# Performance work log

Measured on AMD Instinct MI355X. Metric: run time of the kernel, lower is better.

Reference implementation:

```python
import jax, jax.numpy as jnp
import numpy as np
from jax import lax

B, T = 512, 64
IN, H, V1, P = 256, 512, 101, 8  # input_size, rnn_size, vocab_size+1, max_param
CLS, REG = 512, 512


def setup_inputs() -> dict:
    key = jax.random.key(0)
    ks = jax.random.split(key, 20)
    u = lambda k, s: jax.random.uniform(k, s, jnp.float32, -0.1, 0.1)
    sh = 1.0 / np.sqrt(H)
    ul = lambda k, s: jax.random.uniform(k, s, jnp.float32, -sh, sh)
    return {
        "x": jax.random.normal(ks[0], (B, IN), jnp.float32),
        "y": jax.random.randint(ks[1], (B, T), 0, V1),
        "embed": u(ks[2], (V1, IN)),
        "w_ih0": ul(ks[3], (4 * H, IN)),
        "w_hh0": ul(ks[4], (4 * H, H)),
        "w_ih1": ul(ks[5], (4 * H, H)),
        "w_hh1": ul(ks[6], (4 * H, H)),
        "l1w": u(ks[7], (CLS, H)), "l1b": jnp.zeros((CLS,), jnp.float32),
        "l2w": u(ks[8], (V1, CLS)), "l2b": jnp.zeros((V1,), jnp.float32),
        "r1w": u(ks[9], (REG, H)), "r1b": jnp.zeros((REG,), jnp.float32),
        "r2w": u(ks[10], (V1 * P, V1 + REG)), "r2b": jnp.zeros((V1 * P,), jnp.float32),
    }


def _cell(xi, h, c, wih, whh):
    g = xi @ wih.T + h @ whh.T          # [B, 4H], gate order i,f,g,o (no bias)
    i, f, gg, o = jnp.split(g, 4, axis=-1)
    c = jax.nn.sigmoid(f) * c + jax.nn.sigmoid(i) * jnp.tanh(gg)
    h = jax.nn.sigmoid(o) * jnp.tanh(c)
    return h, c


def reference(x, y, embed, w_ih0, w_hh0, w_ih1, w_hh1,
              l1w, l1b, l2w, l2b, r1w, r1b, r2w, r2b):
    # teacher forcing (sample_prob=0): step-0 input is x, step-i input is embed(y[:, i-1])
    emb = embed[y[:, :-1]]                                  # [B, T-1, IN]
    xt = jnp.concatenate([x[None], jnp.transpose(emb, (1, 0, 2))], axis=0)  # [T, B, IN]

    z = jnp.zeros((x.shape[0], H), x.dtype)

    def step(carry, xi):
        h0, c0, h1, c1 = carry
        h0, c0 = _cell(xi, h0, c0, w_ih0, w_hh0)
        h1, c1 = _cell(h0, h1, c1, w_ih1, w_hh1)
        return (h0, c0, h1, c1), h1

    _, outs = lax.scan(step, (z, z, z, z), xt)              # [T, B, H]

    feat2 = jax.nn.relu(outs @ l1w.T + l1b) @ l2w.T + l2b   # [T, B, V1]
    pgm_score = jax.nn.log_softmax(feat2, axis=-1)
    trans_prob = lax.stop_gradient(jax.nn.softmax(feat2, axis=-1))
    pf1 = jax.nn.relu(outs @ r1w.T + r1b)                   # [T, B, REG]
    ps = (jnp.concatenate([trans_prob, pf1], axis=-1) @ r2w.T + r2b)
    ps = ps.reshape(T, -1, V1, P)                           # [T, B, V1, P]
    idx = y.T                                               # [T, B]
    param = ps[jnp.arange(T)[:, None], jnp.arange(x.shape[0])[None, :], idx]  # [T, B, P]
    return (jnp.transpose(pgm_score, (1, 0, 2)),            # [B, T, V1]
            jnp.transpose(param, (1, 0, 2)))                # [B, T, P]
```

## Files before the change

### kernel.cpp

```cpp
#include <hip/hip_runtime.h>
#include <stdint.h>

typedef unsigned short u16;
typedef short bf16x8 __attribute__((ext_vector_type(8)));
typedef float f32x4 __attribute__((ext_vector_type(4)));
typedef int i32x4 __attribute__((ext_vector_type(4)));

#define DEV static __device__ __forceinline__

constexpr int B_ = 512, T_ = 64, IN_ = 256, H_ = 512, V1_ = 101, P_ = 8, G4_ = 2048;
constexpr int EXR = 613;
constexpr int M_  = T_ * B_;
constexpr int NBLK = 256;

DEV float b2f(u16 u) { union { uint32_t i; float f; } v; v.i = ((uint32_t)u) << 16; return v.f; }
DEV u16 f2b(float f) {
  union { float f; uint32_t i; } v; v.f = f;
  uint32_t i = v.i;
  return (u16)((i + 0x7fffu + ((i >> 16) & 1u)) >> 16);
}
DEV float sigf(float x) { return 1.f / (1.f + __expf(-x)); }
DEV float tanh_(float x) {
  float c = fminf(fmaxf(x, -15.f), 15.f);
  float e = __expf(2.f * c);
  return (e - 1.f) / (e + 1.f);
}
DEV bf16x8 ld8(const u16* p) { return *reinterpret_cast<const bf16x8*>(p); }
DEV f32x4 mfma16(bf16x8 a, bf16x8 b, f32x4 c) {
  return __builtin_amdgcn_mfma_f32_16x16x32_bf16(a, b, c, 0, 0, 0);
}

struct CvtArgs {
  const float* src[9];
  u16* dst[9];
  int pre[10];
};

__global__ __launch_bounds__(256) void k_cvtall(CvtArgs a) {
  int gid = blockIdx.x * 256 + threadIdx.x;
  if (gid >= a.pre[9]) return;
  int s = 0;
#pragma unroll
  for (int i = 1; i < 9; ++i) s += (gid >= a.pre[i]);
  const int local = gid - a.pre[s];
  const float4 v = reinterpret_cast<const float4*>(a.src[s])[local];
  ushort4 o;
  o.x = f2b(v.x); o.y = f2b(v.y); o.z = f2b(v.z); o.w = f2b(v.w);
  reinterpret_cast<ushort4*>(a.dst[s])[local] = o;
}

__global__ __launch_bounds__(256) void k_precomp(const u16* __restrict__ ex_src,
                                                 const u16* __restrict__ wih0b,
                                                 float* __restrict__ EX0) {
  const int lane = threadIdx.x & 63;
  const int wv = threadIdx.x >> 6;
  const int m0 = blockIdx.x * 64 + wv * 16;
  const int n0 = blockIdx.y * 64;
  const int lr = lane & 15;
  const int lk = (lane >> 4) * 8;

  const int arow = m0 + lr;
  const bool valid = arow < EXR;

  f32x4 acc[4] = {};
  for (int k0 = 0; k0 < IN_; k0 += 32) {
    bf16x8 a = {};
    if (valid) a = ld8(ex_src + (size_t)arow * IN_ + k0 + lk);
#pragma unroll
    for (int c = 0; c < 4; ++c) {
      bf16x8 b = ld8(wih0b + (size_t)(n0 + c * 16 + lr) * IN_ + k0 + lk);
      acc[c] = mfma16(a, b, acc[c]);
    }
  }
  const int rb = (lane >> 4) * 4;
#pragma unroll
  for (int c = 0; c < 4; ++c)
#pragma unroll
    for (int r = 0; r < 4; ++r) {
      int row = m0 + rb + r;
      int col = n0 + c * 16 + (lane & 15);
      if (row < EXR) EX0[(size_t)row * G4_ + col] = acc[c][r];
    }
}

__global__ __launch_bounds__(512, 1) void k_scan(
    const u16* __restrict__ whh0, const u16* __restrict__ wih1, const u16* __restrict__ whh1,
    const float* __restrict__ EX0, const int* __restrict__ y,
    u16* h0buf, u16* h1buf, unsigned* flags ) {
  __shared__ u16 h0s[16 * 512];
  __shared__ u16 h1s[16 * 512];
  __shared__ u16 stage0[16][64];
  __shared__ u16 stage1[16][64];
  const size_t BH = (size_t)B_ * H_;
  const int tid = threadIdx.x;
  const int lane = tid & 63;
  const int wv = tid >> 6;
  const int q = wv & 3;
  const bool isL1 = wv >= 4;
  const int bm = blockIdx.x >> 3;
  const int bj = blockIdx.x & 7;
  const int lr = lane & 15;
  const int lk = (lane >> 4) * 8;
  const int col = bj * 64 + q * 16 + lr;
  const int rb = (lane >> 4) * 4;
  const int lcol = q * 16 + lr;

  const u16* wp[8];
#pragma unroll
  for (int g = 0; g < 4; ++g) {
    if (!isL1) {
      wp[g] = whh0 + (size_t)(g * H_ + col) * H_ + lk;
      wp[4 + g] = whh0 + (size_t)(g * H_ + col) * H_ + lk;
    } else {
      wp[g] = wih1 + (size_t)(g * H_ + col) * H_ + lk;
      wp[4 + g] = whh1 + (size_t)(g * H_ + col) * H_ + lk;
    }
  }
  f32x4 cst = {};
  unsigned* gflags = flags + bm * 16;

  for (int k = 0; k <= T_; ++k) {
    {
      const u16* h0g = h0buf + (size_t)k * BH + (size_t)(bm * 16) * H_;
#pragma unroll
      for (int rr = 0; rr < 2; ++rr) {
        const int idx = rr * 512 + tid;
        const int row = idx >> 6, cc = idx & 63;
        i32x4 d = *(const i32x4*)(h0g + (size_t)row * H_ + cc * 8);
        *(i32x4*)((char*)h0s + row * 1024 + ((cc * 16) ^ ((row & 7) << 4))) = d;
      }
      if (k >= 1) {
        const u16* h1g = h1buf + (size_t)(k - 1) * BH + (size_t)(bm * 16) * H_;
#pragma unroll
        for (int rr = 0; rr < 2; ++rr) {
          const int idx = rr * 512 + tid;
          const int row = idx >> 6, cc = idx & 63;
          i32x4 d = *(const i32x4*)(h1g + (size_t)row * H_ + cc * 8);
          *(i32x4*)((char*)h1s + row * 1024 + ((cc * 16) ^ ((row & 7) << 4))) = d;
        }
      }
    }
    __syncthreads();

    if (!isL1) {
      if (k < T_) {
        float ex[4][4];
#pragma unroll
        for (int r = 0; r < 4; ++r) {
          const int row = bm * 16 + rb + r;
          const int srow = (k == 0) ? (V1_ + row) : y[row * T_ + k - 1];
          const float* bp = EX0 + (size_t)srow * G4_ + col;
#pragma unroll
          for (int g = 0; g < 4; ++g) ex[g][r] = bp[(size_t)g * H_];
        }
        bf16x8 wf0[4], wf1[4], wf2[4];
#pragma unroll
        for (int g = 0; g < 4; ++g) {
          wf0[g] = ld8(wp[g]);
          wf1[g] = ld8(wp[g] + 32);
          wf2[g] = ld8(wp[g] + 64);
        }
        f32x4 acc[4] = {};
#pragma unroll
        for (int i = 0; i < 16; ++i) {
          bf16x8 a0 = *(const bf16x8*)((const char*)h0s + lr * 1024 + (((i * 32 + lk) * 2) ^ ((lr & 7) << 4)));
          bf16x8 cur[4];
#pragma unroll
          for (int g = 0; g < 4; ++g)
            cur[g] = (i % 3 == 0) ? wf0[g] : (i % 3 == 1) ? wf1[g] : wf2[g];
          if (i + 3 < 16) {
#pragma unroll
            for (int g = 0; g < 4; ++g) {
              bf16x8 nv = ld8(wp[g] + (i + 3) * 32);
              if (i % 3 == 0) wf0[g] = nv; else if (i % 3 == 1) wf1[g] = nv; else wf2[g] = nv;
            }
          }
#pragma unroll
          for (int g = 0; g < 4; ++g) acc[g] = mfma16(a0, cur[g], acc[g]);
        }
#pragma unroll
        for (int r = 0; r < 4; ++r) {
          float iv = acc[0][r] + ex[0][r], fv = acc[1][r] + ex[1][r];
          float gv = acc[2][r] + ex[2][r], ov = acc[3][r] + ex[3][r];
          float cn = sigf(fv) * cst[r] + sigf(iv) * tanh_(gv);
          cst[r] = cn;
          stage0[rb + r][lcol] = f2b(sigf(ov) * tanh_(cn));
        }
      }
    } else {
      if (k >= 1) {
        bf16x8 wa0[4], wa1[4], wa2[4], wb0[4], wb1[4], wb2[4];
#pragma unroll
        for (int g = 0; g < 4; ++g) {
          wa0[g] = ld8(wp[g]);       wb0[g] = ld8(wp[4 + g]);
          wa1[g] = ld8(wp[g] + 32);  wb1[g] = ld8(wp[4 + g] + 32);
          wa2[g] = ld8(wp[g] + 64);  wb2[g] = ld8(wp[4 + g] + 64);
        }
        f32x4 acc[4] = {};
#pragma unroll
        for (int i = 0; i < 16; ++i) {
          const int so = ((i * 32 + lk) * 2) ^ ((lr & 7) << 4);
          bf16x8 a0 = *(const bf16x8*)((const char*)h0s + lr * 1024 + so);
          bf16x8 a1 = *(const bf16x8*)((const char*)h1s + lr * 1024 + so);
          bf16x8 ca[4], cb[4];
#pragma unroll
          for (int g = 0; g < 4; ++g) {
            ca[g] = (i % 3 == 0) ? wa0[g] : (i % 3 == 1) ? wa1[g] : wa2[g];
            cb[g] = (i % 3 == 0) ? wb0[g] : (i % 3 == 1) ? wb1[g] : wb2[g];
          }
          if (i + 3 < 16) {
#pragma unroll
            for (int g = 0; g < 4; ++g) {
              bf16x8 na = ld8(wp[g] + (i + 3) * 32);
              bf16x8 nb = ld8(wp[4 + g] + (i + 3) * 32);
              if (i % 3 == 0) { wa0[g] = na; wb0[g] = nb; }
              else if (i % 3 == 1) { wa1[g] = na; wb1[g] = nb; }
              else { wa2[g] = na; wb2[g] = nb; }
            }
          }
#pragma unroll
          for (int g = 0; g < 4; ++g) {
            acc[g] = mfma16(a0, ca[g], acc[g]);
            acc[g] = mfma16(a1, cb[g], acc[g]);
          }
        }
#pragma unroll
        for (int r = 0; r < 4; ++r) {
          float cn = sigf(acc[1][r]) * cst[r] + sigf(acc[0][r]) * tanh_(acc[2][r]);
          cst[r] = cn;
          stage1[rb + r][lcol] = f2b(sigf(acc[3][r]) * tanh_(cn));
        }
      }
    }
    __syncthreads();

    if (tid < 256) {
      if (tid < 128) {
        if (k < T_) {
          const int lrow = tid >> 3, c8 = (tid & 7) * 8;
          i32x4 d = *(const i32x4*)&stage0[lrow][c8];
          u16* gp = h0buf + (size_t)(k + 1) * BH + (size_t)(bm * 16 + lrow) * H_ + bj * 64 + c8;
          asm volatile("global_store_dwordx4 %0, %1, off sc0 sc1" :: "v"(gp), "v"(d) : "memory");
        }
      } else {
        if (k >= 1) {
          const int t2 = tid - 128;
          const int lrow = t2 >> 3, c8 = (t2 & 7) * 8;
          i32x4 d = *(const i32x4*)&stage1[lrow][c8];
          u16* gp = h1buf + (size_t)k * BH + (size_t)(bm * 16 + lrow) * H_ + bj * 64 + c8;
          asm volatile("global_store_dwordx4 %0, %1, off sc0 sc1" :: "v"(gp), "v"(d) : "memory");
        }
      }
    }
    asm volatile("s_waitcnt vmcnt(0)" ::: "memory");
    __syncthreads();
    if (wv == 0) {
      const unsigned tgt = (unsigned)(k + 1);
      if (lane == 0)
        __hip_atomic_store(&gflags[bj], tgt, __ATOMIC_RELAXED, __HIP_MEMORY_SCOPE_AGENT);
      for (;;) {
        unsigned v = __hip_atomic_load(&gflags[lane & 7], __ATOMIC_RELAXED, __HIP_MEMORY_SCOPE_AGENT);
        if (__all(v >= tgt)) break;
        __builtin_amdgcn_s_sleep(1);
      }
    }
    __syncthreads();
    asm volatile("" ::: "memory");
  }
}

__global__ __launch_bounds__(256) void k_fused1(const u16* __restrict__ outs,
                                                const u16* __restrict__ l1w, const float* __restrict__ l1b,
                                                const u16* __restrict__ r1w, const float* __restrict__ r1b,
                                                u16* __restrict__ feat1, u16* __restrict__ pf1) {
  const int lane = threadIdx.x & 63;
  const int wv = threadIdx.x >> 6;
  const int lr = lane & 15;
  const int lk = (lane >> 4) * 8;
  const int ar = blockIdx.x * 64 + wv * 16 + lr;
  const int rb = (lane >> 4) * 4;
  const int row0 = blockIdx.x * 64 + wv * 16 + rb;

  bf16x8 a[16];
  {
    const u16* ap = outs + (size_t)ar * H_ + lk;
#pragma unroll
    for (int i = 0; i < 16; ++i) a[i] = ld8(ap + i * 32);
  }
  for (int w = 0; w < 2; ++w) {
    const u16* W = w ? r1w : l1w;
    const float* bias = w ? r1b : l1b;
    u16* dst = w ? pf1 : feat1;
    for (int nc = 0; nc < 4; ++nc) {
      const u16* wr[8];
#pragma unroll
      for (int n = 0; n < 8; ++n)
        wr[n] = W + (size_t)(nc * 128 + n * 16 + lr) * H_ + lk;
      bf16x8 wcur[8];
#pragma unroll
      for (int n = 0; n < 8; ++n) wcur[n] = ld8(wr[n]);
      f32x4 acc[8] = {};
#pragma unroll
      for (int i = 0; i < 16; ++i) {
        bf16x8 wnext[8];
        if (i < 15) {
#pragma unroll
          for (int n = 0; n < 8; ++n) wnext[n] = ld8(wr[n] + (i + 1) * 32);
        }
#pragma unroll
        for (int n = 0; n < 8; ++n) acc[n] = mfma16(a[i], wcur[n], acc[n]);
        if (i < 15) {
#pragma unroll
          for (int n = 0; n < 8; ++n) wcur[n] = wnext[n];
        }
      }
#pragma unroll
      for (int n = 0; n < 8; ++n) {
        const int colc = nc * 128 + n * 16 + lr;
        const float bv = bias[colc];
#pragma unroll
        for (int r = 0; r < 4; ++r)
          dst[(size_t)(row0 + r) * H_ + colc] = f2b(fmaxf(acc[n][r] + bv, 0.f));
      }
    }
  }
}

__global__ __launch_bounds__(256) void k_fused2(const u16* __restrict__ feat1,
                                                const u16* __restrict__ l2w, const float* __restrict__ l2b,
                                                const u16* __restrict__ pf1,
                                                const float* __restrict__ r2w, const float* __restrict__ r2b,
                                                const int* __restrict__ y,
                                                float* __restrict__ pgm, float* __restrict__ par) {
  __shared__ float trans[64][104];
  const int lane = threadIdx.x & 63;
  const int wv = threadIdx.x >> 6;
  const int lr = lane & 15;
  const int lk = (lane >> 4) * 8;
  const int ar = blockIdx.x * 64 + wv * 16 + lr;
  const int rb = (lane >> 4) * 4;

  f32x4 acc[7] = {};
  {
    const u16* ap = feat1 + (size_t)ar * H_ + lk;
#pragma unroll
    for (int i = 0; i < 16; ++i) {
      bf16x8 av = ld8(ap + i * 32);
#pragma unroll
      for (int c = 0; c < 7; ++c) {
        const int n = c * 16 + lr;
        bf16x8 b = {};
        if (n < V1_) b = ld8(l2w + (size_t)n * H_ + i * 32 + lk);
        acc[c] = mfma16(av, b, acc[c]);
      }
    }
  }
#pragma unroll
  for (int r = 0; r < 4; ++r) {
    float v[7];
    float mx = -1e30f;
#pragma unroll
    for (int c = 0; c < 7; ++c) {
      const int colc = c * 16 + lr;
      v[c] = (colc < V1_) ? acc[c][r] + l2b[colc] : -1e30f;
      mx = fmaxf(mx, v[c]);
    }
#pragma unroll
    for (int o = 1; o < 16; o <<= 1) mx = fmaxf(mx, __shfl_xor(mx, o, 64));
    float e[7], s = 0.f;
#pragma unroll
    for (int c = 0; c < 7; ++c) { e[c] = (c * 16 + lr < V1_) ? __expf(v[c] - mx) : 0.f; s += e[c]; }
#pragma unroll
    for (int o = 1; o < 16; o <<= 1) s += __shfl_xor(s, o, 64);
    const float lz = __logf(s), inv = 1.f / s;
    const int m = blockIdx.x * 64 + wv * 16 + rb + r;
    const int t = m >> 9, bb = m & 511;
    float* po = pgm + ((size_t)bb * T_ + t) * V1_;
#pragma unroll
    for (int c = 0; c < 7; ++c) {
      const int colc = c * 16 + lr;
      if (colc < V1_) { po[colc] = v[c] - mx - lz; trans[wv * 16 + rb + r][colc] = e[c] * inv; }
    }
  }
  __syncthreads();
  for (int rr = 0; rr < 16; ++rr) {
    const int m = blockIdx.x * 64 + wv * 16 + rr;
    const int t = m >> 9, bb = m & 511;
    const int idx = y[bb * T_ + t];
    const float* wb = r2w + (size_t)idx * P_ * 613;
    float a8[P_] = {};
    for (int kk = lane; kk < 613; kk += 64) {
      float xv = (kk < V1_) ? trans[wv * 16 + rr][kk] : b2f(pf1[(size_t)m * H_ + kk - V1_]);
#pragma unroll
      for (int p = 0; p < P_; ++p) a8[p] += xv * wb[(size_t)p * 613 + kk];
    }
#pragma unroll
    for (int p = 0; p < P_; ++p)
#pragma unroll
      for (int o = 1; o < 64; o <<= 1) a8[p] += __shfl_xor(a8[p], o, 64);
    if (lane < P_) par[((size_t)bb * T_ + t) * P_ + lane] = a8[lane] + r2b[idx * P_ + lane];
  }
}

extern "C" void kernel_launch(void* const* d_in, const int* in_sizes, int n_in,
                              void* d_out, int out_size, void* d_ws, size_t ws_size,
                              hipStream_t stream) {
  (void)in_sizes; (void)n_in; (void)out_size; (void)ws_size;
  const float* x     = (const float*)d_in[0];
  const int*   y     = (const int*)d_in[1];
  const float* embed = (const float*)d_in[2];
  const float* wih0  = (const float*)d_in[3];
  const float* whh0  = (const float*)d_in[4];
  const float* wih1  = (const float*)d_in[5];
  const float* whh1  = (const float*)d_in[6];
  const float* l1w   = (const float*)d_in[7];
  const float* l1b   = (const float*)d_in[8];
  const float* l2w   = (const float*)d_in[9];
  const float* l2b   = (const float*)d_in[10];
  const float* r1w   = (const float*)d_in[11];
  const float* r1b   = (const float*)d_in[12];
  const float* r2w   = (const float*)d_in[13];
  const float* r2b   = (const float*)d_in[14];

  float* out_pgm = (float*)d_out;
  float* out_par = out_pgm + (size_t)B_ * T_ * V1_;

  char* ws = (char*)d_ws;
  size_t off = 0;
  auto alloc = [&](size_t bytes) { void* p = ws + off; off += (bytes + 255) & ~(size_t)255; return p; };

  const size_t BH2 = (size_t)B_ * H_ * 2;

  unsigned* flags = (unsigned*)alloc(32 * 16 * 4);
  u16* h0buf  = (u16*)alloc((size_t)(T_ + 1) * BH2);
  u16* h1buf  = (u16*)alloc((size_t)(T_ + 1) * BH2);

  float* EX0   = (float*)alloc((size_t)EXR * G4_ * 4);
  u16* ex_src  = (u16*)alloc((size_t)EXR * IN_ * 2);
  u16* wih0b   = (u16*)alloc((size_t)4 * H_ * IN_ * 2);
  u16* whh0b   = (u16*)alloc((size_t)4 * H_ * H_ * 2);
  u16* wih1b   = (u16*)alloc((size_t)4 * H_ * H_ * 2);
  u16* whh1b   = (u16*)alloc((size_t)4 * H_ * H_ * 2);
  u16* l1wb    = (u16*)alloc((size_t)H_ * H_ * 2);
  u16* r1wb    = (u16*)alloc((size_t)H_ * H_ * 2);
  u16* l2wb    = (u16*)alloc((size_t)V1_ * H_ * 2);
  u16* feat1   = (u16*)alloc((size_t)M_ * H_ * 2);
  u16* pf1     = (u16*)alloc((size_t)M_ * H_ * 2);

  (void)hipMemsetAsync(flags, 0, 32 * 16 * 4 + BH2, stream);
  (void)hipMemsetAsync(h1buf, 0, BH2, stream);

  CvtArgs ca;
  const float* srcs[9] = {embed, x, wih0, whh0, wih1, whh1, l1w, r1w, l2w};
  u16* dsts[9] = {ex_src, ex_src + (size_t)V1_ * IN_, wih0b, whh0b, wih1b, whh1b, l1wb, r1wb, l2wb};
  int ns[9] = {V1_ * IN_, B_ * IN_, 4 * H_ * IN_, 4 * H_ * H_, 4 * H_ * H_, 4 * H_ * H_,
               H_ * H_, H_ * H_, V1_ * H_};
  int acc4 = 0;
  for (int i = 0; i < 9; ++i) {
    ca.src[i] = srcs[i]; ca.dst[i] = dsts[i]; ca.pre[i] = acc4; acc4 += ns[i] / 4;
  }
  ca.pre[9] = acc4;
  k_cvtall<<<(acc4 + 255) / 256, 256, 0, stream>>>(ca);

  k_precomp<<<dim3(10, 32), 256, 0, stream>>>(ex_src, wih0b, EX0);

  k_scan<<<NBLK, 512, 0, stream>>>(whh0b, wih1b, whh1b, EX0, y, h0buf, h1buf, flags);

  u16* outs = h1buf + (size_t)B_ * H_;
  k_fused1<<<512, 256, 0, stream>>>(outs, l1wb, l1b, r1wb, r1b, feat1, pf1);
  k_fused2<<<512, 256, 0, stream>>>(feat1, l2wb, l2b, pf1, r2w, r2b, y, out_pgm, out_par);
}
```

Before: 1.934 ms.

## Fuse tail MLP kernels and keep intermediates in swizzled shared memory

Merges the two post-scan kernels into one, so the ReLU hidden features for the classifier and regressor branches stay in LDS instead of going through global memory. XOR swizzling on the LDS rows is meant to avoid bank conflicts when the MFMA loads read them back. This removes one kernel launch and the global write and read of two 32K×512 bf16 buffers. In exchange it uses 128KB of LDS per block, which limits occupancy to one block per CU.

```diff
diff --git a/kernel.cpp b/kernel.cpp
--- a/kernel.cpp
+++ b/kernel.cpp
@@ -269,17 +269,23 @@
   }
 }
 
-__global__ __launch_bounds__(256) void k_fused1(const u16* __restrict__ outs,
-                                                const u16* __restrict__ l1w, const float* __restrict__ l1b,
-                                                const u16* __restrict__ r1w, const float* __restrict__ r1b,
-                                                u16* __restrict__ feat1, u16* __restrict__ pf1) {
+__global__ __launch_bounds__(256) void k_tail(
+    const u16* __restrict__ outs,
+    const u16* __restrict__ l1w, const float* __restrict__ l1b,
+    const u16* __restrict__ r1w, const float* __restrict__ r1b,
+    const u16* __restrict__ l2w, const float* __restrict__ l2b,
+    const float* __restrict__ r2w, const float* __restrict__ r2b,
+    const int* __restrict__ y,
+    float* __restrict__ pgm, float* __restrict__ par) {
+  __shared__ u16 f1s[64 * 512];
+  __shared__ u16 pfs[64 * 512];
   const int lane = threadIdx.x & 63;
   const int wv = threadIdx.x >> 6;
   const int lr = lane & 15;
   const int lk = (lane >> 4) * 8;
-  const int ar = blockIdx.x * 64 + wv * 16 + lr;
   const int rb = (lane >> 4) * 4;
-  const int row0 = blockIdx.x * 64 + wv * 16 + rb;
+  const int lrow0 = wv * 16;
+  const int ar = blockIdx.x * 64 + lrow0 + lr;
 
   bf16x8 a[16];
   {
@@ -287,10 +293,11 @@
 #pragma unroll
     for (int i = 0; i < 16; ++i) a[i] = ld8(ap + i * 32);
   }
+
   for (int w = 0; w < 2; ++w) {
     const u16* W = w ? r1w : l1w;
     const float* bias = w ? r1b : l1b;
-    u16* dst = w ? pf1 : feat1;
+    u16* dst = w ? pfs : f1s;
     for (int nc = 0; nc < 4; ++nc) {
       const u16* wr[8];
 #pragma unroll
@@ -319,42 +326,35 @@
         const int colc = nc * 128 + n * 16 + lr;
         const float bv = bias[colc];
 #pragma unroll
-        for (int r = 0; r < 4; ++r)
-          dst[(size_t)(row0 + r) * H_ + colc] = f2b(fmaxf(acc[n][r] + bv, 0.f));
-      }
-    }
-  }
-}
-
-__global__ __launch_bounds__(256) void k_fused2(const u16* __restrict__ feat1,
-                                                const u16* __restrict__ l2w, const float* __restrict__ l2b,
-                                                const u16* __restrict__ pf1,
-                                                const float* __restrict__ r2w, const float* __restrict__ r2b,
-                                                const int* __restrict__ y,
-                                                float* __restrict__ pgm, float* __restrict__ par) {
-  __shared__ float trans[64][104];
-  const int lane = threadIdx.x & 63;
-  const int wv = threadIdx.x >> 6;
-  const int lr = lane & 15;
-  const int lk = (lane >> 4) * 8;
-  const int ar = blockIdx.x * 64 + wv * 16 + lr;
-  const int rb = (lane >> 4) * 4;
-
-  f32x4 acc[7] = {};
+        for (int r = 0; r < 4; ++r) {
+          const int row = lrow0 + rb + r;
+          *(u16*)((char*)dst + row * 1024 + ((colc * 2) ^ ((row & 7) << 4))) =
+              f2b(fmaxf(acc[n][r] + bv, 0.f));
+        }
+      }
+    }
+  }
+  __syncthreads();
+
+  f32x4 acc2[7] = {};
   {
-    const u16* ap = feat1 + (size_t)ar * H_ + lk;
+    const int arow = lrow0 + lr;
 #pragma unroll
     for (int i = 0; i < 16; ++i) {
-      bf16x8 av = ld8(ap + i * 32);
+      bf16x8 av = *(const bf16x8*)((const char*)f1s + arow * 1024 +
+                                   (((i * 32 + lk) * 2) ^ ((arow & 7) << 4)));
 #pragma unroll
       for (int c = 0; c < 7; ++c) {
         const int n = c * 16 + lr;
         bf16x8 b = {};
         if (n < V1_) b = ld8(l2w + (size_t)n * H_ + i * 32 + lk);
-        acc[c] = mfma16(av, b, acc[c]);
-      }
-    }
-  }
+        acc2[c] = mfma16(av, b, acc2[c]);
+      }
+    }
+  }
+  __syncthreads();
+  float* trans = (float*)f1s;
+
 #pragma unroll
   for (int r = 0; r < 4; ++r) {
     float v[7];
@@ -362,7 +362,7 @@
 #pragma unroll
     for (int c = 0; c < 7; ++c) {
       const int colc = c * 16 + lr;
-      v[c] = (colc < V1_) ? acc[c][r] + l2b[colc] : -1e30f;
+      v[c] = (colc < V1_) ? acc2[c][r] + l2b[colc] : -1e30f;
       mx = fmaxf(mx, v[c]);
     }
 #pragma unroll
@@ -373,24 +373,32 @@
 #pragma unroll
     for (int o = 1; o < 16; o <<= 1) s += __shfl_xor(s, o, 64);
     const float lz = __logf(s), inv = 1.f / s;
-    const int m = blockIdx.x * 64 + wv * 16 + rb + r;
+    const int lrow = lrow0 + rb + r;
+    const int m = blockIdx.x * 64 + lrow;
     const int t = m >> 9, bb = m & 511;
     float* po = pgm + ((size_t)bb * T_ + t) * V1_;
 #pragma unroll
     for (int c = 0; c < 7; ++c) {
       const int colc = c * 16 + lr;
-      if (colc < V1_) { po[colc] = v[c] - mx - lz; trans[wv * 16 + rb + r][colc] = e[c] * inv; }
+      if (colc < V1_) { po[colc] = v[c] - mx - lz; trans[lrow * 104 + colc] = e[c] * inv; }
     }
   }
   __syncthreads();
+
   for (int rr = 0; rr < 16; ++rr) {
-    const int m = blockIdx.x * 64 + wv * 16 + rr;
+    const int lrow = wv * 16 + rr;
+    const int m = blockIdx.x * 64 + lrow;
     const int t = m >> 9, bb = m & 511;
     const int idx = y[bb * T_ + t];
     const float* wb = r2w + (size_t)idx * P_ * 613;
     float a8[P_] = {};
     for (int kk = lane; kk < 613; kk += 64) {
-      float xv = (kk < V1_) ? trans[wv * 16 + rr][kk] : b2f(pf1[(size_t)m * H_ + kk - V1_]);
+      float xv;
+      if (kk < V1_) xv = trans[lrow * 104 + kk];
+      else {
+        const int cc = kk - V1_;
+        xv = b2f(*(const u16*)((const char*)pfs + lrow * 1024 + ((cc * 2) ^ ((lrow & 7) << 4))));
+      }
 #pragma unroll
       for (int p = 0; p < P_; ++p) a8[p] += xv * wb[(size_t)p * 613 + kk];
     }
@@ -444,8 +452,6 @@
   u16* l1wb    = (u16*)alloc((size_t)H_ * H_ * 2);
   u16* r1wb    = (u16*)alloc((size_t)H_ * H_ * 2);
   u16* l2wb    = (u16*)alloc((size_t)V1_ * H_ * 2);
-  u16* feat1   = (u16*)alloc((size_t)M_ * H_ * 2);
-  u16* pf1     = (u16*)alloc((size_t)M_ * H_ * 2);
 
   (void)hipMemsetAsync(flags, 0, 32 * 16 * 4 + BH2, stream);
   (void)hipMemsetAsync(h1buf, 0, BH2, stream);
@@ -467,6 +473,6 @@
   k_scan<<<NBLK, 512, 0, stream>>>(whh0b, wih1b, whh1b, EX0, y, h0buf, h1buf, flags);
 
   u16* outs = h1buf + (size_t)B_ * H_;
-  k_fused1<<<512, 256, 0, stream>>>(outs, l1wb, l1b, r1wb, r1b, feat1, pf1);
-  k_fused2<<<512, 256, 0, stream>>>(feat1, l2wb, l2b, pf1, r2w, r2b, y, out_pgm, out_par);
-}
+  k_tail<<<512, 256, 0, stream>>>(outs, l1wb, l1b, r1wb, r1b, l2wb, l2b, r2w, r2b, y,
+                                  out_pgm, out_par);
+}
```

Result: slower. 2.000 ms (+3.5%).
